# Performance work log

Measured on AMD Instinct MI355X. Metric: run time of the kernel, lower is better.

## Reference

```python
import jax, jax.numpy as jnp
import numpy as np
from jax import lax


def _causal_mask(shape, mask_center):
    # shape = (out_ch, in_ch, h, w); mirrors CausalConv2d mask construction
    o, i, h, w = shape
    m = np.zeros(shape, dtype=np.float32)
    m[:, :, : h // 2, :] = 1.0
    m[:, :, h // 2, : w // 2 + (0 if mask_center else 1)] = 1.0
    return jnp.asarray(m)

MASK1 = _causal_mask((16, 1, 7, 7), mask_center=True)
MASK2 = _causal_mask((16, 16, 3, 3), mask_center=False)


def _conv(x, w, b, pad):
    y = lax.conv_general_dilated(
        x, w, window_strides=(1, 1), padding=[(pad, pad), (pad, pad)],
        dimension_numbers=("NCHW", "OIHW", "NCHW"))
    return y + b[None, :, None, None]


def setup_inputs() -> dict:
    key = jax.random.key(0)
    ks = jax.random.split(key, 7)
    B, H, W = 1024, 64, 64
    x = jax.random.uniform(ks[0], (B, 1, H, W), dtype=jnp.float32)
    # Kaiming-ish init scales
    w1 = jax.random.normal(ks[1], (16, 1, 7, 7), jnp.float32) * (1.0 / np.sqrt(1 * 49))
    b1 = jax.random.normal(ks[2], (16,), jnp.float32) * 0.01
    w2 = jax.random.normal(ks[3], (16, 16, 3, 3), jnp.float32) * (1.0 / np.sqrt(16 * 9))
    b2 = jax.random.normal(ks[4], (16,), jnp.float32) * 0.01
    w3 = jax.random.normal(ks[5], (1, 16, 1, 1), jnp.float32) * (1.0 / np.sqrt(16))
    b3 = jax.random.normal(ks[6], (1,), jnp.float32) * 0.01
    return {"x": x, "w1": w1, "b1": b1, "w2": w2, "b2": b2, "w3": w3, "b3": b3}


def reference(x, w1, b1, w2, b2, w3, b3):
    # PixelCNN._forward: masked conv7x7 -> relu -> masked conv3x3 -> relu -> conv1x1 -> sigmoid
    h = jax.nn.relu(_conv(x, w1 * MASK1, b1, pad=3))
    h = jax.nn.relu(_conv(h, w2 * MASK2, b2, pad=1))
    return jax.nn.sigmoid(_conv(h, w3, b3, pad=0))
```

## Files before the change

### kernel.cpp

```cpp
#include <hip/hip_runtime.h>

typedef _Float16 half8  __attribute__((ext_vector_type(8)));
typedef __fp16   fp16x2 __attribute__((ext_vector_type(2)));
typedef float    floatx4 __attribute__((ext_vector_type(4)));

#define IMG_H 64
#define IMG_W 64
#define TH 8
#define INW 72
#define INH 12
#define H1W 66
#define H1H 9
#define PLDW (H1H*H1W*2)
#define CP 912
#define CPM1 911

__device__ __forceinline__ unsigned pk2u(float a, float b) {
    fp16x2 h = __builtin_amdgcn_cvt_pkrtz(a, b);
    return __builtin_bit_cast(unsigned, h);
}

__global__ __launch_bounds__(256, 8) void pixelcnn_mfma11(
    const float* __restrict__ x,
    const float* __restrict__ w1, const float* __restrict__ b1,
    const float* __restrict__ w2, const float* __restrict__ b2,
    const float* __restrict__ w3, const float* __restrict__ b3,
    float* __restrict__ out)
{
    __shared__ __align__(16) _Float16      s16[4 * CP];
    __shared__ __align__(16) _Float16      s_w1t[16 * 32];
    __shared__ __align__(16) unsigned char s_w2t8[16 * 96];
    __shared__ __align__(16) float         s_b1[16], s_b2[16], s_w3[16];
    __shared__ float                       s_b3;
    __shared__ __align__(16) unsigned      s_h1[2 * PLDW];

    const int t    = threadIdx.x;
    const int lane = t & 63;
    const int wave = t >> 6;
    const int n    = lane & 15;
    const int quad = lane >> 4;
    const int img  = blockIdx.y;
    const int ty0  = blockIdx.x * TH;

    const float* xim = x + img * (IMG_H * IMG_W);

    if (t < 216) {
        int r = t / 18, c4 = (t - r * 18) * 4;
        int gy = ty0 - 4 + r;
        int gx0 = c4 - 4;
        float4 v  = {0.f, 0.f, 0.f, 0.f};
        float4 v2 = {0.f, 0.f, 0.f, 0.f};
        if ((unsigned)gy < IMG_H) {
            const float* rp = xim + gy * IMG_W;
            if ((unsigned)gx0 < IMG_W)       v  = *(const float4*)(rp + gx0);
            if ((unsigned)(gx0 + 4) < IMG_W) v2 = *(const float4*)(rp + gx0 + 4);
        }
        unsigned a0 = pk2u(v.x,  v.y),  a1 = pk2u(v.z,  v.w);
        unsigned a2 = pk2u(v2.x, v2.y), a3 = pk2u(v2.z, v2.w);
        unsigned m10 = (a0 >> 16) | (a1 << 16);
        unsigned m21 = (a1 >> 16) | (a2 << 16);
        unsigned m32 = (a2 >> 16) | (a3 << 16);
        int lin = r * INW + c4;
        *(uint2*)&s16[0*CP + 4 + lin] = uint2{a0,  a1 };
        *(uint2*)&s16[1*CP + 4 + lin] = uint2{m10, m21};
        *(uint2*)&s16[2*CP + 4 + lin] = uint2{a1,  a2 };
        *(uint2*)&s16[3*CP + 4 + lin] = uint2{m21, m32};
    } else if (t < 234) {
        int idx = t - 216;
        int cell = (idx >> 1) * H1W + ((idx & 1) ? 65 : 0);
        *(uint2*)&s_h1[cell * 2]        = uint2{0u, 0u};
        *(uint2*)&s_h1[PLDW + cell * 2] = uint2{0u, 0u};
    }
    {
        int ch = t >> 4, l = t & 15;
        const float* w1c = w1 + ch * 49;
#pragma unroll
        for (int j2 = 0; j2 < 2; ++j2) {
            int k = l + 16 * j2, q = k >> 3, jj = k & 7;
            float v = 0.f;
            if (q < 3)      { if (jj < 7) v = w1c[q * 7 + jj]; }
            else            { if (jj < 3) v = w1c[21 + jj];    }
            s_w1t[ch * 32 + k] = (_Float16)v;
        }
        const float* w2cl = w2 + (ch * 16 + l) * 9;
#pragma unroll
        for (int j = 0; j < 6; ++j) {
            float v = (j < 5) ? w2cl[j] : 0.f;
            unsigned q8 = (unsigned)__builtin_amdgcn_cvt_pk_fp8_f32(v, 0.f, 0, false);
            s_w2t8[ch * 96 + j * 16 + l] = (unsigned char)(q8 & 0xff);
        }
    }
    if (t < 16) { s_b1[t] = b1[t]; s_b2[t] = b2[t]; s_w3[t] = w3[t]; }
    if (t == 16) s_b3 = b3[0];
    __syncthreads();

    {
        const half8 afrag = *(const half8*)&s_w1t[n * 32 + quad * 8];
        const floatx4 bias1 = ((const floatx4*)s_b1)[quad];
        const int px = wave * 16 + n;
        const int S  = px + 1;
        const int c  = S & 3;
        const _Float16* ap0 = &s16[c * CPM1 + 4 + S + quad * INW];
        const unsigned wd0 = (unsigned)((quad >> 1) * PLDW + S * 2 + (quad & 1));
        const bool top = (ty0 == 0);

#pragma unroll
        for (int i = 0; i < H1H; ++i) {
            const _Float16* ap = ap0 + i * INW;
            uint2 lo = *(const uint2*)ap;
            uint2 hi = *(const uint2*)(ap + 4);
            uint4 bu; bu.x = lo.x; bu.y = lo.y; bu.z = hi.x; bu.w = hi.y;
            half8 b = __builtin_bit_cast(half8, bu);
            floatx4 acc = bias1;
            acc = __builtin_amdgcn_mfma_f32_16x16x32_f16(afrag, b, acc, 0, 0, 0);
            int d = __builtin_amdgcn_cvt_pk_fp8_f32(fmaxf(acc[0], 0.f), fmaxf(acc[1], 0.f), 0, false);
            d = __builtin_amdgcn_cvt_pk_fp8_f32(fmaxf(acc[2], 0.f), fmaxf(acc[3], 0.f), d, true);
            unsigned dv = (unsigned)d;
            if (i == 0) dv = top ? 0u : dv;
            s_h1[wd0 + i * (H1W * 2)] = dv;
        }
    }
    __syncthreads();

    {
        const long w2f0 = *(const long*)&s_w2t8[n * 96 +  0 + quad * 8];
        const long w2f1 = *(const long*)&s_w2t8[n * 96 + 32 + quad * 8];
        const long w2f2 = *(const long*)&s_w2t8[n * 96 + 64 + quad * 8];
        const floatx4 bias2 = ((const floatx4*)s_b2)[quad];
        const floatx4 w3q   = ((const floatx4*)s_w3)[quad];
        const float bias3 = s_b3;
        const int x0 = wave * 16;
        const int tqh = quad >> 1, plane = quad & 1;
        const int E0 = H1W + x0 + n + 1;
        const char* h1b = (const char*)s_h1 + plane * (PLDW * 4);
        const char* a0 = h1b + (E0 - H1W - 1 + tqh) * 8;
        const char* a1 = h1b + (E0 + (tqh ? -1 : -(H1W - 1))) * 8;
        const char* a2 = h1b + E0 * 8;
        float* sbase = out + ((img * IMG_H) + ty0 + quad) * IMG_W + x0 + n;

#pragma unroll
        for (int g = 0; g < 2; ++g) {
            float sv0, sv1, sv2, sv3;
#pragma unroll
            for (int q = 0; q < 4; ++q) {
                const int k = g * 4 + q;
                floatx4 acc = bias2;
                acc = __builtin_amdgcn_mfma_f32_16x16x32_fp8_fp8(w2f0, *(const long*)(a0 + k * 528), acc, 0, 0, 0);
                acc = __builtin_amdgcn_mfma_f32_16x16x32_fp8_fp8(w2f1, *(const long*)(a1 + k * 528), acc, 0, 0, 0);
                acc = __builtin_amdgcn_mfma_f32_16x16x32_fp8_fp8(w2f2, *(const long*)(a2 + k * 528), acc, 0, 0, 0);
                float s = fmaxf(acc[0], 0.f) * w3q[0];
                s = fmaf(fmaxf(acc[1], 0.f), w3q[1], s);
                s = fmaf(fmaxf(acc[2], 0.f), w3q[2], s);
                s = fmaf(fmaxf(acc[3], 0.f), w3q[3], s);
                s += __shfl_xor(s, 16);
                s += __shfl_xor(s, 32);
                if      (q == 0) sv0 = s;
                else if (q == 1) sv1 = s;
                else if (q == 2) sv2 = s;
                else             sv3 = s;
            }
            float t01 = (quad & 1) ? sv1 : sv0;
            float t23 = (quad & 1) ? sv3 : sv2;
            float v   = (quad & 2) ? t23 : t01;
            float r = __builtin_amdgcn_rcpf(1.f + __expf(-(v + bias3)));
            *(float*)((char*)sbase + g * 1024) = r;
        }
    }
}

extern "C" void kernel_launch(void* const* d_in, const int* in_sizes, int n_in,
                              void* d_out, int out_size, void* d_ws, size_t ws_size,
                              hipStream_t stream) {
    const float* x  = (const float*)d_in[0];
    const float* w1 = (const float*)d_in[1];
    const float* b1 = (const float*)d_in[2];
    const float* w2 = (const float*)d_in[3];
    const float* b2 = (const float*)d_in[4];
    const float* w3 = (const float*)d_in[5];
    const float* b3 = (const float*)d_in[6];
    float* out = (float*)d_out;

    dim3 grid(8, 1024);
    dim3 block(256);
    hipLaunchKernelGGL(pixelcnn_mfma11, grid, block, 0, stream,
                       x, w1, b1, w2, b2, w3, b3, out);
}
```

Baseline: 105.1 us.

## Double row tile to 16 with 512-thread blocks and load conv1 weights into registers

Measured after the change: 101.2 us. 3.6% less time.

```diff
diff --git a/kernel.cpp b/kernel.cpp
--- a/kernel.cpp
+++ b/kernel.cpp
@@ -3,35 +3,33 @@
 typedef _Float16 half8  __attribute__((ext_vector_type(8)));
 typedef __fp16   fp16x2 __attribute__((ext_vector_type(2)));
 typedef float    floatx4 __attribute__((ext_vector_type(4)));
+typedef float    f4a __attribute__((ext_vector_type(4), aligned(4)));
 
 #define IMG_H 64
 #define IMG_W 64
-#define TH 8
+#define TH 16
 #define INW 72
-#define INH 12
 #define H1W 66
-#define H1H 9
+#define H1H 17
 #define PLDW (H1H*H1W*2)
-#define CP 912
-#define CPM1 911
+#define CP 1440
+#define CPM1 1439
+#define S16N (4*CP + 4)
 
 __device__ __forceinline__ unsigned pk2u(float a, float b) {
     fp16x2 h = __builtin_amdgcn_cvt_pkrtz(a, b);
     return __builtin_bit_cast(unsigned, h);
 }
 
-__global__ __launch_bounds__(256, 8) void pixelcnn_mfma11(
+__global__ __launch_bounds__(512, 8) void pixelcnn_mfma12(
     const float* __restrict__ x,
     const float* __restrict__ w1, const float* __restrict__ b1,
     const float* __restrict__ w2, const float* __restrict__ b2,
     const float* __restrict__ w3, const float* __restrict__ b3,
     float* __restrict__ out)
 {
-    __shared__ __align__(16) _Float16      s16[4 * CP];
-    __shared__ __align__(16) _Float16      s_w1t[16 * 32];
+    __shared__ __align__(16) _Float16      s16[S16N];
     __shared__ __align__(16) unsigned char s_w2t8[16 * 96];
-    __shared__ __align__(16) float         s_b1[16], s_b2[16], s_w3[16];
-    __shared__ float                       s_b3;
     __shared__ __align__(16) unsigned      s_h1[2 * PLDW];
 
     const int t    = threadIdx.x;
@@ -39,12 +37,34 @@
     const int wave = t >> 6;
     const int n    = lane & 15;
     const int quad = lane >> 4;
+    const int s    = wave >> 2;
+    const int x0q  = wave & 3;
     const int img  = blockIdx.y;
     const int ty0  = blockIdx.x * TH;
 
     const float* xim = x + img * (IMG_H * IMG_W);
 
-    if (t < 216) {
+    const float* wr = w1 + n * 49 + quad * 7;
+    f4a wlo = *(const f4a*)wr;
+    f4a whi = *(const f4a*)(wr + 3);
+    const floatx4 bias1 = *(const floatx4*)(b1 + quad * 4);
+    const floatx4 bias2 = *(const floatx4*)(b2 + quad * 4);
+    const floatx4 w3q   = *(const floatx4*)(w3 + quad * 4);
+    const float   bias3 = b3[0];
+    half8 af;
+    {
+        bool q3 = (quad == 3);
+        af[0] = (_Float16)wlo[0];
+        af[1] = (_Float16)wlo[1];
+        af[2] = (_Float16)wlo[2];
+        af[3] = (_Float16)(q3 ? 0.f : wlo[3]);
+        af[4] = (_Float16)(q3 ? 0.f : whi[1]);
+        af[5] = (_Float16)(q3 ? 0.f : whi[2]);
+        af[6] = (_Float16)(q3 ? 0.f : whi[3]);
+        af[7] = (_Float16)0.f;
+    }
+
+    if (t < 360) {
         int r = t / 18, c4 = (t - r * 18) * 4;
         int gy = ty0 - 4 + r;
         int gx0 = c4 - 4;
@@ -65,23 +85,14 @@
         *(uint2*)&s16[1*CP + 4 + lin] = uint2{m10, m21};
         *(uint2*)&s16[2*CP + 4 + lin] = uint2{a1,  a2 };
         *(uint2*)&s16[3*CP + 4 + lin] = uint2{m21, m32};
-    } else if (t < 234) {
-        int idx = t - 216;
+    } else if (t < 394) {
+        int idx = t - 360;
         int cell = (idx >> 1) * H1W + ((idx & 1) ? 65 : 0);
         *(uint2*)&s_h1[cell * 2]        = uint2{0u, 0u};
         *(uint2*)&s_h1[PLDW + cell * 2] = uint2{0u, 0u};
     }
-    {
-        int ch = t >> 4, l = t & 15;
-        const float* w1c = w1 + ch * 49;
-#pragma unroll
-        for (int j2 = 0; j2 < 2; ++j2) {
-            int k = l + 16 * j2, q = k >> 3, jj = k & 7;
-            float v = 0.f;
-            if (q < 3)      { if (jj < 7) v = w1c[q * 7 + jj]; }
-            else            { if (jj < 3) v = w1c[21 + jj];    }
-            s_w1t[ch * 32 + k] = (_Float16)v;
-        }
+    if (t >= 256) {
+        int ch = (t >> 4) & 15, l = t & 15;
         const float* w2cl = w2 + (ch * 16 + l) * 9;
 #pragma unroll
         for (int j = 0; j < 6; ++j) {
@@ -90,33 +101,30 @@
             s_w2t8[ch * 96 + j * 16 + l] = (unsigned char)(q8 & 0xff);
         }
     }
-    if (t < 16) { s_b1[t] = b1[t]; s_b2[t] = b2[t]; s_w3[t] = w3[t]; }
-    if (t == 16) s_b3 = b3[0];
     __syncthreads();
 
     {
-        const half8 afrag = *(const half8*)&s_w1t[n * 32 + quad * 8];
-        const floatx4 bias1 = ((const floatx4*)s_b1)[quad];
-        const int px = wave * 16 + n;
+        const int px = x0q * 16 + n;
         const int S  = px + 1;
         const int c  = S & 3;
-        const _Float16* ap0 = &s16[c * CPM1 + 4 + S + quad * INW];
-        const unsigned wd0 = (unsigned)((quad >> 1) * PLDW + S * 2 + (quad & 1));
-        const bool top = (ty0 == 0);
+        const _Float16* ap0 = &s16[c * CPM1 + 4 + S + (s * 8 + quad) * INW];
+        const unsigned wd0 = (unsigned)((quad >> 1) * PLDW + ((s * 8) * H1W + S) * 2 + (quad & 1));
+        const bool top = (ty0 == 0) && (s == 0);
 
 #pragma unroll
-        for (int i = 0; i < H1H; ++i) {
+        for (int i = 0; i < 9; ++i) {
+            if (i == 0 && s != 0) continue;
             const _Float16* ap = ap0 + i * INW;
             uint2 lo = *(const uint2*)ap;
             uint2 hi = *(const uint2*)(ap + 4);
             uint4 bu; bu.x = lo.x; bu.y = lo.y; bu.z = hi.x; bu.w = hi.y;
             half8 b = __builtin_bit_cast(half8, bu);
             floatx4 acc = bias1;
-            acc = __builtin_amdgcn_mfma_f32_16x16x32_f16(afrag, b, acc, 0, 0, 0);
+            acc = __builtin_amdgcn_mfma_f32_16x16x32_f16(af, b, acc, 0, 0, 0);
             int d = __builtin_amdgcn_cvt_pk_fp8_f32(fmaxf(acc[0], 0.f), fmaxf(acc[1], 0.f), 0, false);
             d = __builtin_amdgcn_cvt_pk_fp8_f32(fmaxf(acc[2], 0.f), fmaxf(acc[3], 0.f), d, true);
             unsigned dv = (unsigned)d;
-            if (i == 0) dv = top ? 0u : dv;
+            if (i == 0 && top) dv = 0u;
             s_h1[wd0 + i * (H1W * 2)] = dv;
         }
     }
@@ -126,17 +134,14 @@
         const long w2f0 = *(const long*)&s_w2t8[n * 96 +  0 + quad * 8];
         const long w2f1 = *(const long*)&s_w2t8[n * 96 + 32 + quad * 8];
         const long w2f2 = *(const long*)&s_w2t8[n * 96 + 64 + quad * 8];
-        const floatx4 bias2 = ((const floatx4*)s_b2)[quad];
-        const floatx4 w3q   = ((const floatx4*)s_w3)[quad];
-        const float bias3 = s_b3;
-        const int x0 = wave * 16;
+        const int x0 = x0q * 16;
         const int tqh = quad >> 1, plane = quad & 1;
-        const int E0 = H1W + x0 + n + 1;
+        const int E0 = (s * 8 + 1) * H1W + x0 + n + 1;
         const char* h1b = (const char*)s_h1 + plane * (PLDW * 4);
         const char* a0 = h1b + (E0 - H1W - 1 + tqh) * 8;
         const char* a1 = h1b + (E0 + (tqh ? -1 : -(H1W - 1))) * 8;
         const char* a2 = h1b + E0 * 8;
-        float* sbase = out + ((img * IMG_H) + ty0 + quad) * IMG_W + x0 + n;
+        float* sbase = out + ((img * IMG_H) + ty0 + s * 8 + quad) * IMG_W + x0 + n;
 
 #pragma unroll
         for (int g = 0; g < 2; ++g) {
@@ -148,16 +153,16 @@
                 acc = __builtin_amdgcn_mfma_f32_16x16x32_fp8_fp8(w2f0, *(const long*)(a0 + k * 528), acc, 0, 0, 0);
                 acc = __builtin_amdgcn_mfma_f32_16x16x32_fp8_fp8(w2f1, *(const long*)(a1 + k * 528), acc, 0, 0, 0);
                 acc = __builtin_amdgcn_mfma_f32_16x16x32_fp8_fp8(w2f2, *(const long*)(a2 + k * 528), acc, 0, 0, 0);
-                float s = fmaxf(acc[0], 0.f) * w3q[0];
-                s = fmaf(fmaxf(acc[1], 0.f), w3q[1], s);
-                s = fmaf(fmaxf(acc[2], 0.f), w3q[2], s);
-                s = fmaf(fmaxf(acc[3], 0.f), w3q[3], s);
-                s += __shfl_xor(s, 16);
-                s += __shfl_xor(s, 32);
-                if      (q == 0) sv0 = s;
-                else if (q == 1) sv1 = s;
-                else if (q == 2) sv2 = s;
-                else             sv3 = s;
+                float sacc = fmaxf(acc[0], 0.f) * w3q[0];
+                sacc = fmaf(fmaxf(acc[1], 0.f), w3q[1], sacc);
+                sacc = fmaf(fmaxf(acc[2], 0.f), w3q[2], sacc);
+                sacc = fmaf(fmaxf(acc[3], 0.f), w3q[3], sacc);
+                sacc += __shfl_xor(sacc, 16);
+                sacc += __shfl_xor(sacc, 32);
+                if      (q == 0) sv0 = sacc;
+                else if (q == 1) sv1 = sacc;
+                else if (q == 2) sv2 = sacc;
+                else             sv3 = sacc;
             }
             float t01 = (quad & 1) ? sv1 : sv0;
             float t23 = (quad & 1) ? sv3 : sv2;
@@ -180,8 +185,8 @@
     const float* b3 = (const float*)d_in[6];
     float* out = (float*)d_out;
 
-    dim3 grid(8, 1024);
-    dim3 block(256);
-    hipLaunchKernelGGL(pixelcnn_mfma11, grid, block, 0, stream,
+    dim3 grid(4, 1024);
+    dim3 block(512);
+    hipLaunchKernelGGL(pixelcnn_mfma12, grid, block, 0, stream,
                        x, w1, b1, w2, b2, w3, b3, out);
 }
```
